# Performance work log

Measured on AMD Instinct MI355X. Metric: run time of the kernel, lower is better.

Reference implementation:

```python
import jax, jax.numpy as jnp
import numpy as np

N = 50000
IN_CH = 256
HID = 256
E = 800000


def setup_inputs() -> dict:
    key = jax.random.key(0)
    ks = jax.random.split(key, 12)
    s = 1.0 / np.sqrt(HID)
    return {
        "x": jax.random.normal(ks[0], (N, IN_CH), jnp.float32),
        "edge_index": jax.random.randint(ks[1], (2, E), 0, N, dtype=jnp.int64),
        "prev_embedding": jax.random.normal(ks[2], (N, HID), jnp.float32),
        "W1": jax.random.normal(ks[3], (IN_CH, HID), jnp.float32) / np.sqrt(IN_CH),
        "b1": jnp.zeros((HID,), jnp.float32),
        "W2": jax.random.normal(ks[4], (HID, HID), jnp.float32) * s,
        "b2": jnp.zeros((HID,), jnp.float32),
        "gWw": jax.random.normal(ks[5], (HID, HID), jnp.float32) * s,
        "gWb": jnp.zeros((HID,), jnp.float32),
        "gUw": jax.random.normal(ks[6], (HID, HID), jnp.float32) * s,
        "gUb": jnp.zeros((HID,), jnp.float32),
    }


def _gcn_conv(x, W, b, src, dst, norm):
    # PyG GCNConv: h = x @ W; out[i] = sum_j norm_ij * h[j]; + bias
    h = x @ W
    msg = h[src] * norm[:, None]  # [E+N, H]
    out = jax.ops.segment_sum(msg, dst, num_segments=N)
    return out + b


def _norm_and_loops(edge_index):
    loop = jnp.arange(N, dtype=edge_index.dtype)
    src = jnp.concatenate([edge_index[0], loop])
    dst = jnp.concatenate([edge_index[1], loop])
    deg = jax.ops.segment_sum(jnp.ones_like(dst, dtype=jnp.float32), dst, num_segments=N)
    dinv = jnp.where(deg > 0, jax.lax.rsqrt(deg), 0.0)
    norm = dinv[src] * dinv[dst]
    return src, dst, norm


def reference(x, edge_index, prev_embedding, W1, b1, W2, b2, gWw, gWb, gUw, gUb):
    src, dst, norm = _norm_and_loops(edge_index)
    h = jax.nn.relu(_gcn_conv(x, W1, b1, src, dst, norm))
    h_t = _gcn_conv(h, W2, b2, src, dst, norm)
    alpha = jax.nn.sigmoid(h_t @ gWw + gWb + prev_embedding @ gUw + gUb)
    h_tilde = alpha * h_t + (1.0 - alpha) * prev_embedding
    return (h_tilde, h_t)
```

## Files before the change

kernel.cpp:

```cpp
#include <hip/hip_runtime.h>
#include <hip/hip_bf16.h>
#include <math.h>

#define HIDC 256
#define LSTR 40

typedef short short8 __attribute__((ext_vector_type(8)));
typedef float f32x4 __attribute__((ext_vector_type(4)));

__device__ __forceinline__ ushort f2bf_rne(float f) {
    uint u = __float_as_uint(f);
    u += 0x7FFF + ((u >> 16) & 1);
    return (ushort)(u >> 16);
}
__device__ __forceinline__ float bf2f(ushort h) {
    return __uint_as_float(((uint)h) << 16);
}


__global__ void fill_i_kernel(int* __restrict__ p, int v, int n) {
    int i = blockIdx.x * 256 + threadIdx.x;
    if (i < n) p[i] = v;
}

__global__ void deg_kernel(const int* __restrict__ dst, int* __restrict__ deg, int E) {
    int e = blockIdx.x * 256 + threadIdx.x;
    if (e < E) atomicAdd(&deg[dst[e]], 1);
}

__global__ void rsqrt_kernel(const int* __restrict__ deg, float* __restrict__ dinv, int n) {
    int i = blockIdx.x * 256 + threadIdx.x;
    if (i < n) dinv[i] = rsqrtf((float)(deg[i] + 1));
}


__device__ __forceinline__ int block_incl_scan(int v, int tid) {
#pragma unroll
    for (int off = 1; off < 64; off <<= 1) {
        int t = __shfl_up(v, off);
        if ((tid & 63) >= off) v += t;
    }
    __shared__ int wt[4];
    if ((tid & 63) == 63) wt[tid >> 6] = v;
    __syncthreads();
    int wid = tid >> 6;
    for (int w = 0; w < wid; w++) v += wt[w];
    __syncthreads();
    return v;
}

__global__ void scan_a_kernel(const int* __restrict__ deg, int* __restrict__ row_start,
                              int* __restrict__ blocksum, int N) {
    int tid = threadIdx.x;
    int i = blockIdx.x * 256 + tid;
    int v = (i < N) ? deg[i] : 0;
    int incl = block_incl_scan(v, tid);
    if (i < N) row_start[i + 1] = incl;
    if (tid == 255) blocksum[blockIdx.x] = incl;
}

__global__ void scan_b_kernel(int* __restrict__ blocksum, int nb) {
    int tid = threadIdx.x;
    int v = (tid < nb) ? blocksum[tid] : 0;
    int incl = block_incl_scan(v, tid);
    if (tid < nb) blocksum[tid] = incl;
}

__global__ void scan_c_kernel(int* __restrict__ row_start, int* __restrict__ cursor,
                              const int* __restrict__ blocksum, int N) {
    int b = blockIdx.x;
    int i = b * 256 + threadIdx.x;
    int add = (b > 0) ? blocksum[b - 1] : 0;
    if (i < N) {
        int v = row_start[i + 1] + add;
        row_start[i + 1] = v;
        cursor[i + 1] = v;
    }
    if (b == 0 && threadIdx.x == 0) { row_start[0] = 0; cursor[0] = 0; }
}

__global__ void scatter_kernel(const int* __restrict__ src, const int* __restrict__ dst,
                               const float* __restrict__ dinv, int* __restrict__ cursor,
                               int* __restrict__ csr_src, float* __restrict__ csr_w, int E) {
    int e = blockIdx.x * 256 + threadIdx.x;
    if (e < E) {
        int s = src[e], d = dst[e];
        int pos = atomicAdd(&cursor[d], 1);
        csr_src[pos] = s;
        csr_w[pos] = dinv[s] * dinv[d];
    }
}


__global__ void prep_bt_kernel(const float* __restrict__ B, ushort* __restrict__ Bt) {
    int n = blockIdx.x, k = threadIdx.x;
    Bt[n * 256 + k] = f2bf_rne(B[k * 256 + n]);
}

__global__ void prep_gate_bt_kernel(const float* __restrict__ gWw, const float* __restrict__ gUw,
                                    ushort* __restrict__ Bth, ushort* __restrict__ Btl) {
    int n = blockIdx.x, k = threadIdx.x;
    float v1 = gWw[k * 256 + n];
    uint u1 = __float_as_uint(v1);
    Bth[n * 512 + k] = (ushort)(u1 >> 16);
    Btl[n * 512 + k] = f2bf_rne(v1 - __uint_as_float(u1 & 0xFFFF0000u));
    float v2 = gUw[k * 256 + n];
    uint u2 = __float_as_uint(v2);
    Bth[n * 512 + 256 + k] = (ushort)(u2 >> 16);
    Btl[n * 512 + 256 + k] = f2bf_rne(v2 - __uint_as_float(u2 & 0xFFFF0000u));
}


__global__ __launch_bounds__(256, 4) void gemm_bf16_kernel(
    const float* __restrict__ A, const ushort* __restrict__ Bt,
    ushort* __restrict__ C, int M)
{
    __shared__ __align__(16) ushort As[128 * LSTR];
    __shared__ __align__(16) ushort Bs[128 * LSTR];
    const int tl = threadIdx.x;
    const int lane = tl & 63, wave = tl >> 6;
    const int wm = (wave & 1) * 64, wn = (wave >> 1) * 64;
    const int bm = blockIdx.x * 128, bn = blockIdx.y * 128;

    const int ar  = tl >> 1;
    const int akq = (tl & 1) * 16;
    const bool aok = (bm + ar) < M;

    f32x4 acc[4][4] = {};

    for (int k0 = 0; k0 < 256; k0 += 32) {
        {
            const float* ap = A + (size_t)(bm + ar) * HIDC + k0 + akq;
#pragma unroll
            for (int j = 0; j < 4; j++) {
                float4 v = aok ? *(const float4*)(ap + 4 * j) : make_float4(0.f, 0.f, 0.f, 0.f);
                ushort4 h;
                h.x = f2bf_rne(v.x); h.y = f2bf_rne(v.y);
                h.z = f2bf_rne(v.z); h.w = f2bf_rne(v.w);
                *(ushort4*)&As[ar * LSTR + akq + 4 * j] = h;
            }
        }
        {
            const ushort* bp = Bt + (size_t)(bn + ar) * 256 + k0 + akq;
            *(uint4*)&Bs[ar * LSTR + akq]     = *(const uint4*)bp;
            *(uint4*)&Bs[ar * LSTR + akq + 8] = *(const uint4*)(bp + 8);
        }
        __syncthreads();
        const int fr = lane & 15, koff = (lane >> 4) * 8;
        short8 af[4], bfv[4];
#pragma unroll
        for (int t = 0; t < 4; t++) {
            af[t]  = *(const short8*)&As[(wm + t * 16 + fr) * LSTR + koff];
            bfv[t] = *(const short8*)&Bs[(wn + t * 16 + fr) * LSTR + koff];
        }
#pragma unroll
        for (int mt = 0; mt < 4; mt++)
#pragma unroll
            for (int nt = 0; nt < 4; nt++)
                acc[mt][nt] = __builtin_amdgcn_mfma_f32_16x16x32_bf16(af[mt], bfv[nt], acc[mt][nt], 0, 0, 0);
        __syncthreads();
    }

    const int row4 = (lane >> 4) * 4, coln = lane & 15;
#pragma unroll
    for (int mt = 0; mt < 4; mt++)
#pragma unroll
        for (int r = 0; r < 4; r++) {
            int m = bm + wm + mt * 16 + row4 + r;
            if (m < M) {
#pragma unroll
                for (int nt = 0; nt < 4; nt++) {
                    int n = bn + wn + nt * 16 + coln;
                    C[(size_t)m * HIDC + n] = f2bf_rne(acc[mt][nt][r]);
                }
            }
        }
}


__global__ __launch_bounds__(256, 4) void gemm_bf16A_kernel(
    const ushort* __restrict__ A, const ushort* __restrict__ Bt,
    ushort* __restrict__ C, int M)
{
    __shared__ __align__(16) ushort As[128 * LSTR];
    __shared__ __align__(16) ushort Bs[128 * LSTR];
    const int tl = threadIdx.x;
    const int lane = tl & 63, wave = tl >> 6;
    const int wm = (wave & 1) * 64, wn = (wave >> 1) * 64;
    const int bm = blockIdx.x * 128, bn = blockIdx.y * 128;

    const int ar  = tl >> 1;
    const int akq = (tl & 1) * 16;
    const bool aok = (bm + ar) < M;

    f32x4 acc[4][4] = {};

    for (int k0 = 0; k0 < 256; k0 += 32) {
        {
            const ushort* ap = A + (size_t)(bm + ar) * HIDC + k0 + akq;
            uint4 z = make_uint4(0u, 0u, 0u, 0u);
            *(uint4*)&As[ar * LSTR + akq]     = aok ? *(const uint4*)ap       : z;
            *(uint4*)&As[ar * LSTR + akq + 8] = aok ? *(const uint4*)(ap + 8) : z;
        }
        {
            const ushort* bp = Bt + (size_t)(bn + ar) * 256 + k0 + akq;
            *(uint4*)&Bs[ar * LSTR + akq]     = *(const uint4*)bp;
            *(uint4*)&Bs[ar * LSTR + akq + 8] = *(const uint4*)(bp + 8);
        }
        __syncthreads();
        const int fr = lane & 15, koff = (lane >> 4) * 8;
        short8 af[4], bfv[4];
#pragma unroll
        for (int t = 0; t < 4; t++) {
            af[t]  = *(const short8*)&As[(wm + t * 16 + fr) * LSTR + koff];
            bfv[t] = *(const short8*)&Bs[(wn + t * 16 + fr) * LSTR + koff];
        }
#pragma unroll
        for (int mt = 0; mt < 4; mt++)
#pragma unroll
            for (int nt = 0; nt < 4; nt++)
                acc[mt][nt] = __builtin_amdgcn_mfma_f32_16x16x32_bf16(af[mt], bfv[nt], acc[mt][nt], 0, 0, 0);
        __syncthreads();
    }

    const int row4 = (lane >> 4) * 4, coln = lane & 15;
#pragma unroll
    for (int mt = 0; mt < 4; mt++)
#pragma unroll
        for (int r = 0; r < 4; r++) {
            int m = bm + wm + mt * 16 + row4 + r;
            if (m < M) {
#pragma unroll
                for (int nt = 0; nt < 4; nt++) {
                    int n = bn + wn + nt * 16 + coln;
                    C[(size_t)m * HIDC + n] = f2bf_rne(acc[mt][nt][r]);
                }
            }
        }
}


__global__ __launch_bounds__(256, 4) void gate_kernel(
    const float* __restrict__ ht, const float* __restrict__ prev,
    const ushort* __restrict__ Bth, const ushort* __restrict__ Btl,
    const float* __restrict__ gWb, const float* __restrict__ gUb,
    float* __restrict__ out, int M)
{
    __shared__ __align__(16) ushort Ash[64 * LSTR];
    __shared__ __align__(16) ushort Asl[64 * LSTR];
    __shared__ __align__(16) ushort Bsh[128 * LSTR];
    __shared__ __align__(16) ushort Bsl[128 * LSTR];
    const int tl = threadIdx.x;
    const int lane = tl & 63, wave = tl >> 6;
    const int wm = (wave & 1) * 32, wn = (wave >> 1) * 64;
    const int bm = blockIdx.x * 64, bn = blockIdx.y * 128;

    const int arA = tl >> 2;
    const int kqA = (tl & 3) * 8;
    const int arB = tl >> 1;
    const int kqB = (tl & 1) * 16;
    const bool aok = (bm + arA) < M;

    f32x4 acc[2][4] = {};

    for (int k0 = 0; k0 < 512; k0 += 32) {
        {
            const float* srcA = (k0 < 256) ? ht : prev;
            const float* ap = srcA + (size_t)(bm + arA) * HIDC + (k0 & 255) + kqA;
            float4 v0 = aok ? *(const float4*)(ap)     : make_float4(0.f, 0.f, 0.f, 0.f);
            float4 v1 = aok ? *(const float4*)(ap + 4) : make_float4(0.f, 0.f, 0.f, 0.f);
            float vv[8] = {v0.x, v0.y, v0.z, v0.w, v1.x, v1.y, v1.z, v1.w};
            ushort hp[8], lp[8];
#pragma unroll
            for (int q = 0; q < 8; q++) {
                uint u = __float_as_uint(vv[q]);
                hp[q] = (ushort)(u >> 16);
                lp[q] = f2bf_rne(vv[q] - __uint_as_float(u & 0xFFFF0000u));
            }
            *(ushort4*)&Ash[arA * LSTR + kqA]     = make_ushort4(hp[0], hp[1], hp[2], hp[3]);
            *(ushort4*)&Ash[arA * LSTR + kqA + 4] = make_ushort4(hp[4], hp[5], hp[6], hp[7]);
            *(ushort4*)&Asl[arA * LSTR + kqA]     = make_ushort4(lp[0], lp[1], lp[2], lp[3]);
            *(ushort4*)&Asl[arA * LSTR + kqA + 4] = make_ushort4(lp[4], lp[5], lp[6], lp[7]);
        }
        {
            const ushort* bph = Bth + (size_t)(bn + arB) * 512 + k0 + kqB;
            const ushort* bpl = Btl + (size_t)(bn + arB) * 512 + k0 + kqB;
            *(uint4*)&Bsh[arB * LSTR + kqB]     = *(const uint4*)bph;
            *(uint4*)&Bsh[arB * LSTR + kqB + 8] = *(const uint4*)(bph + 8);
            *(uint4*)&Bsl[arB * LSTR + kqB]     = *(const uint4*)bpl;
            *(uint4*)&Bsl[arB * LSTR + kqB + 8] = *(const uint4*)(bpl + 8);
        }
        __syncthreads();
        const int fr = lane & 15, koff = (lane >> 4) * 8;
        short8 afh[2], afl[2], bfh[4], bfl[4];
#pragma unroll
        for (int t = 0; t < 2; t++) {
            afh[t] = *(const short8*)&Ash[(wm + t * 16 + fr) * LSTR + koff];
            afl[t] = *(const short8*)&Asl[(wm + t * 16 + fr) * LSTR + koff];
        }
#pragma unroll
        for (int t = 0; t < 4; t++) {
            bfh[t] = *(const short8*)&Bsh[(wn + t * 16 + fr) * LSTR + koff];
            bfl[t] = *(const short8*)&Bsl[(wn + t * 16 + fr) * LSTR + koff];
        }
#pragma unroll
        for (int mt = 0; mt < 2; mt++)
#pragma unroll
            for (int nt = 0; nt < 4; nt++) {
                acc[mt][nt] = __builtin_amdgcn_mfma_f32_16x16x32_bf16(afh[mt], bfh[nt], acc[mt][nt], 0, 0, 0);
                acc[mt][nt] = __builtin_amdgcn_mfma_f32_16x16x32_bf16(afh[mt], bfl[nt], acc[mt][nt], 0, 0, 0);
                acc[mt][nt] = __builtin_amdgcn_mfma_f32_16x16x32_bf16(afl[mt], bfh[nt], acc[mt][nt], 0, 0, 0);
            }
        __syncthreads();
    }

    const int row4 = (lane >> 4) * 4, coln = lane & 15;
#pragma unroll
    for (int mt = 0; mt < 2; mt++)
#pragma unroll
        for (int r = 0; r < 4; r++) {
            int m = bm + wm + mt * 16 + row4 + r;
            if (m < M) {
#pragma unroll
                for (int nt = 0; nt < 4; nt++) {
                    int n = bn + wn + nt * 16 + coln;
                    size_t idx = (size_t)m * HIDC + n;
                    float g = acc[mt][nt][r] + gWb[n] + gUb[n];
                    float alpha = 1.f / (1.f + expf(-g));
                    out[idx] = alpha * ht[idx] + (1.f - alpha) * prev[idx];
                }
            }
        }
}


__global__ __launch_bounds__(256) void csr_agg_kernel(
    const ushort* __restrict__ hm, const int* __restrict__ row_start,
    const int* __restrict__ csr_src, const float* __restrict__ csr_w,
    const float* __restrict__ dinv, const float* __restrict__ bias,
    float* __restrict__ outf, ushort* __restrict__ outb, int do_relu, int N)
{
    const int wave = threadIdx.x >> 6, lane = threadIdx.x & 63;
    const int i = blockIdx.x * 4 + wave;
    if (i >= N) return;
    const int c = lane * 4;

    const float di = dinv[i];
    const float s2 = di * di;
    ushort4 sv = *(const ushort4*)(hm + (size_t)i * HIDC + c);
    float a0 = s2 * bf2f(sv.x), a1 = s2 * bf2f(sv.y);
    float a2 = s2 * bf2f(sv.z), a3 = s2 * bf2f(sv.w);

    const int b0 = row_start[i], b1 = row_start[i + 1];
    int t = b0;
    for (; t + 4 <= b1; t += 4) {
        int   i0 = csr_src[t],     i1 = csr_src[t + 1];
        int   i2 = csr_src[t + 2], i3 = csr_src[t + 3];
        float w0 = csr_w[t],       w1 = csr_w[t + 1];
        float w2 = csr_w[t + 2],   w3 = csr_w[t + 3];
        ushort4 v0 = *(const ushort4*)(hm + (size_t)i0 * HIDC + c);
        ushort4 v1 = *(const ushort4*)(hm + (size_t)i1 * HIDC + c);
        ushort4 v2 = *(const ushort4*)(hm + (size_t)i2 * HIDC + c);
        ushort4 v3 = *(const ushort4*)(hm + (size_t)i3 * HIDC + c);
        a0 += w0 * bf2f(v0.x); a1 += w0 * bf2f(v0.y); a2 += w0 * bf2f(v0.z); a3 += w0 * bf2f(v0.w);
        a0 += w1 * bf2f(v1.x); a1 += w1 * bf2f(v1.y); a2 += w1 * bf2f(v1.z); a3 += w1 * bf2f(v1.w);
        a0 += w2 * bf2f(v2.x); a1 += w2 * bf2f(v2.y); a2 += w2 * bf2f(v2.z); a3 += w2 * bf2f(v2.w);
        a0 += w3 * bf2f(v3.x); a1 += w3 * bf2f(v3.y); a2 += w3 * bf2f(v3.z); a3 += w3 * bf2f(v3.w);
    }
    for (; t < b1; ++t) {
        int s_ = csr_src[t];
        float w = csr_w[t];
        ushort4 v = *(const ushort4*)(hm + (size_t)s_ * HIDC + c);
        a0 += w * bf2f(v.x); a1 += w * bf2f(v.y); a2 += w * bf2f(v.z); a3 += w * bf2f(v.w);
    }

    float4 bb = *(const float4*)(bias + c);
    a0 += bb.x; a1 += bb.y; a2 += bb.z; a3 += bb.w;
    if (do_relu) {
        a0 = fmaxf(a0, 0.f); a1 = fmaxf(a1, 0.f);
        a2 = fmaxf(a2, 0.f); a3 = fmaxf(a3, 0.f);
    }
    if (outb) {
        ushort4 o;
        o.x = f2bf_rne(a0); o.y = f2bf_rne(a1);
        o.z = f2bf_rne(a2); o.w = f2bf_rne(a3);
        *(ushort4*)(outb + (size_t)i * HIDC + c) = o;
    } else {
        *(float4*)(outf + (size_t)i * HIDC + c) = make_float4(a0, a1, a2, a3);
    }
}


extern "C" void kernel_launch(void* const* d_in, const int* in_sizes, int n_in,
                              void* d_out, int out_size, void* d_ws, size_t ws_size,
                              hipStream_t stream) {
    const float* x    = (const float*)d_in[0];
    const int*   ei   = (const int*)d_in[1];
    const float* prev = (const float*)d_in[2];
    const float* W1   = (const float*)d_in[3];
    const float* b1   = (const float*)d_in[4];
    const float* W2   = (const float*)d_in[5];
    const float* b2   = (const float*)d_in[6];
    const float* gWw  = (const float*)d_in[7];
    const float* gWb  = (const float*)d_in[8];
    const float* gUw  = (const float*)d_in[9];
    const float* gUb  = (const float*)d_in[10];

    const int N = in_sizes[0] / HIDC;
    const int E = in_sizes[1] / 2;
    const int* src = ei;
    const int* dst = ei + E;

    float* out  = (float*)d_out;
    float* out1 = out;
    float* ht   = out + (size_t)N * HIDC;
    ushort* hbf = (ushort*)out1;

    float* ws = (float*)d_ws;
    size_t o = 0;
    auto take = [&](size_t n) { size_t r = o; o += (n + 63) & ~(size_t)63; return r; };
    float*  dinv    = ws + take(N);
    int*    degi    = (int*)(ws + take(N));
    int*    row_st  = (int*)(ws + take(N + 1));
    int*    cursor  = (int*)(ws + take(N + 1));
    int*    csr_src = (int*)(ws + take(E));
    float*  csr_w   = ws + take(E);
    ushort* Bt1     = (ushort*)(ws + take(256 * 256 / 2));
    ushort* Bt2     = (ushort*)(ws + take(256 * 256 / 2));
    ushort* Bth     = (ushort*)(ws + take(256 * 512 / 2));
    ushort* Btl     = (ushort*)(ws + take(256 * 512 / 2));
    ushort* hm      = (ushort*)(ws + take((size_t)N * HIDC / 2));

    const int nbN = (N + 255) / 256;
    const int nbE = (E + 255) / 256;
    dim3 ggrid((N + 127) / 128, 2);
    dim3 ggridG((N + 63) / 64, 2);
    const int nbAgg = (N + 3) / 4;

    int* blocksum = (int*)csr_w;
    fill_i_kernel<<<nbN, 256, 0, stream>>>(degi, 0, N);
    deg_kernel<<<nbE, 256, 0, stream>>>(dst, degi, E);
    scan_a_kernel<<<nbN, 256, 0, stream>>>(degi, row_st, blocksum, N);
    scan_b_kernel<<<1, 256, 0, stream>>>(blocksum, nbN);
    scan_c_kernel<<<nbN, 256, 0, stream>>>(row_st, cursor, blocksum, N);
    rsqrt_kernel<<<nbN, 256, 0, stream>>>(degi, dinv, N);
    scatter_kernel<<<nbE, 256, 0, stream>>>(src, dst, dinv, cursor, csr_src, csr_w, E);

    prep_bt_kernel<<<256, 256, 0, stream>>>(W1, Bt1);
    prep_bt_kernel<<<256, 256, 0, stream>>>(W2, Bt2);
    prep_gate_bt_kernel<<<256, 256, 0, stream>>>(gWw, gUw, Bth, Btl);

    gemm_bf16_kernel<<<ggrid, 256, 0, stream>>>(x, Bt1, hm, N);
    csr_agg_kernel<<<nbAgg, 256, 0, stream>>>(hm, row_st, csr_src, csr_w, dinv, b1,
                                              nullptr, hbf, 1, N);

    gemm_bf16A_kernel<<<ggrid, 256, 0, stream>>>(hbf, Bt2, hm, N);
    csr_agg_kernel<<<nbAgg, 256, 0, stream>>>(hm, row_st, csr_src, csr_w, dinv, b2,
                                              ht, nullptr, 0, N);

    gate_kernel<<<ggridG, 256, 0, stream>>>(ht, prev, Bth, Btl, gWb, gUb, out1, N);

    (void)n_in; (void)out_size; (void)ws_size;
}
```

Measured before the change: 509.2 us.

## Double-buffer LDS in GEMM kernels and fuse small prep/rsqrt kernels

Both bf16 GEMM kernels now use double-buffered shared memory with register prefetch of the next K-slice, so global loads overlap MFMA work and each iteration needs only one barrier. The rsqrt degree computation is folded into the scan kernel, and the three weight transpose/convert kernels are merged into a single launch, which cuts launch overhead. The larger LDS footprint lowers the launch-bounds occupancy hint from 4 to 3 blocks.

```diff
diff --git a/kernel.cpp b/kernel.cpp
--- a/kernel.cpp
+++ b/kernel.cpp
@@ -16,6 +16,9 @@
 __device__ __forceinline__ float bf2f(ushort h) {
     return __uint_as_float(((uint)h) << 16);
 }
+__device__ __forceinline__ f32x4 MF(short8 a, short8 b, f32x4 c) {
+    return __builtin_amdgcn_mfma_f32_16x16x32_bf16(a, b, c, 0, 0, 0);
+}
 
 
 __global__ void fill_i_kernel(int* __restrict__ p, int v, int n) {
@@ -26,11 +29,6 @@
 __global__ void deg_kernel(const int* __restrict__ dst, int* __restrict__ deg, int E) {
     int e = blockIdx.x * 256 + threadIdx.x;
     if (e < E) atomicAdd(&deg[dst[e]], 1);
-}
-
-__global__ void rsqrt_kernel(const int* __restrict__ deg, float* __restrict__ dinv, int n) {
-    int i = blockIdx.x * 256 + threadIdx.x;
-    if (i < n) dinv[i] = rsqrtf((float)(deg[i] + 1));
 }
 
 
@@ -50,12 +48,15 @@
 }
 
 __global__ void scan_a_kernel(const int* __restrict__ deg, int* __restrict__ row_start,
-                              int* __restrict__ blocksum, int N) {
+                              int* __restrict__ blocksum, float* __restrict__ dinv, int N) {
     int tid = threadIdx.x;
     int i = blockIdx.x * 256 + tid;
     int v = (i < N) ? deg[i] : 0;
     int incl = block_incl_scan(v, tid);
-    if (i < N) row_start[i + 1] = incl;
+    if (i < N) {
+        row_start[i + 1] = incl;
+        dinv[i] = rsqrtf((float)(v + 1));
+    }
     if (tid == 255) blocksum[blockIdx.x] = incl;
 }
 
@@ -92,14 +93,13 @@
 }
 
 
-__global__ void prep_bt_kernel(const float* __restrict__ B, ushort* __restrict__ Bt) {
+__global__ void prep_all_kernel(const float* __restrict__ W1, const float* __restrict__ W2,
+                                const float* __restrict__ gWw, const float* __restrict__ gUw,
+                                ushort* __restrict__ Bt1, ushort* __restrict__ Bt2,
+                                ushort* __restrict__ Bth, ushort* __restrict__ Btl) {
     int n = blockIdx.x, k = threadIdx.x;
-    Bt[n * 256 + k] = f2bf_rne(B[k * 256 + n]);
-}
-
-__global__ void prep_gate_bt_kernel(const float* __restrict__ gWw, const float* __restrict__ gUw,
-                                    ushort* __restrict__ Bth, ushort* __restrict__ Btl) {
-    int n = blockIdx.x, k = threadIdx.x;
+    Bt1[n * 256 + k] = f2bf_rne(W1[k * 256 + n]);
+    Bt2[n * 256 + k] = f2bf_rne(W2[k * 256 + n]);
     float v1 = gWw[k * 256 + n];
     uint u1 = __float_as_uint(v1);
     Bth[n * 512 + k] = (ushort)(u1 >> 16);
@@ -111,12 +111,12 @@
 }
 
 
-__global__ __launch_bounds__(256, 4) void gemm_bf16_kernel(
+__global__ __launch_bounds__(256, 3) void gemm_bf16_kernel(
     const float* __restrict__ A, const ushort* __restrict__ Bt,
     ushort* __restrict__ C, int M)
 {
-    __shared__ __align__(16) ushort As[128 * LSTR];
-    __shared__ __align__(16) ushort Bs[128 * LSTR];
+    __shared__ __align__(16) ushort As[2][128 * LSTR];
+    __shared__ __align__(16) ushort Bs[2][128 * LSTR];
     const int tl = threadIdx.x;
     const int lane = tl & 63, wave = tl >> 6;
     const int wm = (wave & 1) * 64, wn = (wave >> 1) * 64;
@@ -125,40 +125,63 @@
     const int ar  = tl >> 1;
     const int akq = (tl & 1) * 16;
     const bool aok = (bm + ar) < M;
+    const float*  apb = A  + (size_t)(bm + ar) * HIDC + akq;
+    const ushort* bpb = Bt + (size_t)(bn + ar) * 256 + akq;
 
     f32x4 acc[4][4] = {};
-
-    for (int k0 = 0; k0 < 256; k0 += 32) {
-        {
-            const float* ap = A + (size_t)(bm + ar) * HIDC + k0 + akq;
+    const float4 z4 = make_float4(0.f, 0.f, 0.f, 0.f);
+    float4 ra[4]; uint4 rb0, rb1;
+
+#pragma unroll
+    for (int j = 0; j < 4; j++) ra[j] = aok ? *(const float4*)(apb + 4 * j) : z4;
+    rb0 = *(const uint4*)(bpb);
+    rb1 = *(const uint4*)(bpb + 8);
+#pragma unroll
+    for (int j = 0; j < 4; j++) {
+        ushort4 h;
+        h.x = f2bf_rne(ra[j].x); h.y = f2bf_rne(ra[j].y);
+        h.z = f2bf_rne(ra[j].z); h.w = f2bf_rne(ra[j].w);
+        *(ushort4*)&As[0][ar * LSTR + akq + 4 * j] = h;
+    }
+    *(uint4*)&Bs[0][ar * LSTR + akq]     = rb0;
+    *(uint4*)&Bs[0][ar * LSTR + akq + 8] = rb1;
+    __syncthreads();
+
+    const int fr = lane & 15, koff = (lane >> 4) * 8;
+    int cur = 0;
+#pragma unroll
+    for (int kq = 0; kq < 8; kq++) {
+        if (kq + 1 < 8) {
+#pragma unroll
+            for (int j = 0; j < 4; j++)
+                ra[j] = aok ? *(const float4*)(apb + (kq + 1) * 32 + 4 * j) : z4;
+            rb0 = *(const uint4*)(bpb + (kq + 1) * 32);
+            rb1 = *(const uint4*)(bpb + (kq + 1) * 32 + 8);
+        }
+        short8 af[4], bfv[4];
+#pragma unroll
+        for (int t = 0; t < 4; t++) {
+            af[t]  = *(const short8*)&As[cur][(wm + t * 16 + fr) * LSTR + koff];
+            bfv[t] = *(const short8*)&Bs[cur][(wn + t * 16 + fr) * LSTR + koff];
+        }
+#pragma unroll
+        for (int mt = 0; mt < 4; mt++)
+#pragma unroll
+            for (int nt = 0; nt < 4; nt++)
+                acc[mt][nt] = MF(af[mt], bfv[nt], acc[mt][nt]);
+        if (kq + 1 < 8) {
 #pragma unroll
             for (int j = 0; j < 4; j++) {
-                float4 v = aok ? *(const float4*)(ap + 4 * j) : make_float4(0.f, 0.f, 0.f, 0.f);
                 ushort4 h;
-                h.x = f2bf_rne(v.x); h.y = f2bf_rne(v.y);
-                h.z = f2bf_rne(v.z); h.w = f2bf_rne(v.w);
-                *(ushort4*)&As[ar * LSTR + akq + 4 * j] = h;
+                h.x = f2bf_rne(ra[j].x); h.y = f2bf_rne(ra[j].y);
+                h.z = f2bf_rne(ra[j].z); h.w = f2bf_rne(ra[j].w);
+                *(ushort4*)&As[cur ^ 1][ar * LSTR + akq + 4 * j] = h;
             }
-        }
-        {
-            const ushort* bp = Bt + (size_t)(bn + ar) * 256 + k0 + akq;
-            *(uint4*)&Bs[ar * LSTR + akq]     = *(const uint4*)bp;
-            *(uint4*)&Bs[ar * LSTR + akq + 8] = *(const uint4*)(bp + 8);
-        }
-        __syncthreads();
-        const int fr = lane & 15, koff = (lane >> 4) * 8;
-        short8 af[4], bfv[4];
-#pragma unroll
-        for (int t = 0; t < 4; t++) {
-            af[t]  = *(const short8*)&As[(wm + t * 16 + fr) * LSTR + koff];
-            bfv[t] = *(const short8*)&Bs[(wn + t * 16 + fr) * LSTR + koff];
-        }
-#pragma unroll
-        for (int mt = 0; mt < 4; mt++)
-#pragma unroll
-            for (int nt = 0; nt < 4; nt++)
-                acc[mt][nt] = __builtin_amdgcn_mfma_f32_16x16x32_bf16(af[mt], bfv[nt], acc[mt][nt], 0, 0, 0);
-        __syncthreads();
+            *(uint4*)&Bs[cur ^ 1][ar * LSTR + akq]     = rb0;
+            *(uint4*)&Bs[cur ^ 1][ar * LSTR + akq + 8] = rb1;
+            __syncthreads();
+            cur ^= 1;
+        }
     }
 
     const int row4 = (lane >> 4) * 4, coln = lane & 15;
@@ -178,12 +201,12 @@
 }
 
 
-__global__ __launch_bounds__(256, 4) void gemm_bf16A_kernel(
+__global__ __launch_bounds__(256, 3) void gemm_bf16A_kernel(
     const ushort* __restrict__ A, const ushort* __restrict__ Bt,
     ushort* __restrict__ C, int M)
 {
-    __shared__ __align__(16) ushort As[128 * LSTR];
-    __shared__ __align__(16) ushort Bs[128 * LSTR];
+    __shared__ __align__(16) ushort As[2][128 * LSTR];
+    __shared__ __align__(16) ushort Bs[2][128 * LSTR];
     const int tl = threadIdx.x;
     const int lane = tl & 63, wave = tl >> 6;
     const int wm = (wave & 1) * 64, wn = (wave >> 1) * 64;
@@ -192,35 +215,52 @@
     const int ar  = tl >> 1;
     const int akq = (tl & 1) * 16;
     const bool aok = (bm + ar) < M;
+    const ushort* apb = A  + (size_t)(bm + ar) * HIDC + akq;
+    const ushort* bpb = Bt + (size_t)(bn + ar) * 256 + akq;
 
     f32x4 acc[4][4] = {};
-
-    for (int k0 = 0; k0 < 256; k0 += 32) {
-        {
-            const ushort* ap = A + (size_t)(bm + ar) * HIDC + k0 + akq;
-            uint4 z = make_uint4(0u, 0u, 0u, 0u);
-            *(uint4*)&As[ar * LSTR + akq]     = aok ? *(const uint4*)ap       : z;
-            *(uint4*)&As[ar * LSTR + akq + 8] = aok ? *(const uint4*)(ap + 8) : z;
-        }
-        {
-            const ushort* bp = Bt + (size_t)(bn + ar) * 256 + k0 + akq;
-            *(uint4*)&Bs[ar * LSTR + akq]     = *(const uint4*)bp;
-            *(uint4*)&Bs[ar * LSTR + akq + 8] = *(const uint4*)(bp + 8);
-        }
-        __syncthreads();
-        const int fr = lane & 15, koff = (lane >> 4) * 8;
+    const uint4 z = make_uint4(0u, 0u, 0u, 0u);
+    uint4 ua0, ua1, rb0, rb1;
+
+    ua0 = aok ? *(const uint4*)(apb)     : z;
+    ua1 = aok ? *(const uint4*)(apb + 8) : z;
+    rb0 = *(const uint4*)(bpb);
+    rb1 = *(const uint4*)(bpb + 8);
+    *(uint4*)&As[0][ar * LSTR + akq]     = ua0;
+    *(uint4*)&As[0][ar * LSTR + akq + 8] = ua1;
+    *(uint4*)&Bs[0][ar * LSTR + akq]     = rb0;
+    *(uint4*)&Bs[0][ar * LSTR + akq + 8] = rb1;
+    __syncthreads();
+
+    const int fr = lane & 15, koff = (lane >> 4) * 8;
+    int cur = 0;
+#pragma unroll
+    for (int kq = 0; kq < 8; kq++) {
+        if (kq + 1 < 8) {
+            ua0 = aok ? *(const uint4*)(apb + (kq + 1) * 32)     : z;
+            ua1 = aok ? *(const uint4*)(apb + (kq + 1) * 32 + 8) : z;
+            rb0 = *(const uint4*)(bpb + (kq + 1) * 32);
+            rb1 = *(const uint4*)(bpb + (kq + 1) * 32 + 8);
+        }
         short8 af[4], bfv[4];
 #pragma unroll
         for (int t = 0; t < 4; t++) {
-            af[t]  = *(const short8*)&As[(wm + t * 16 + fr) * LSTR + koff];
-            bfv[t] = *(const short8*)&Bs[(wn + t * 16 + fr) * LSTR + koff];
+            af[t]  = *(const short8*)&As[cur][(wm + t * 16 + fr) * LSTR + koff];
+            bfv[t] = *(const short8*)&Bs[cur][(wn + t * 16 + fr) * LSTR + koff];
         }
 #pragma unroll
         for (int mt = 0; mt < 4; mt++)
 #pragma unroll
             for (int nt = 0; nt < 4; nt++)
-                acc[mt][nt] = __builtin_amdgcn_mfma_f32_16x16x32_bf16(af[mt], bfv[nt], acc[mt][nt], 0, 0, 0);
-        __syncthreads();
+                acc[mt][nt] = MF(af[mt], bfv[nt], acc[mt][nt]);
+        if (kq + 1 < 8) {
+            *(uint4*)&As[cur ^ 1][ar * LSTR + akq]     = ua0;
+            *(uint4*)&As[cur ^ 1][ar * LSTR + akq + 8] = ua1;
+            *(uint4*)&Bs[cur ^ 1][ar * LSTR + akq]     = rb0;
+            *(uint4*)&Bs[cur ^ 1][ar * LSTR + akq + 8] = rb1;
+            __syncthreads();
+            cur ^= 1;
+        }
     }
 
     const int row4 = (lane >> 4) * 4, coln = lane & 15;
@@ -440,15 +480,12 @@
     int* blocksum = (int*)csr_w;
     fill_i_kernel<<<nbN, 256, 0, stream>>>(degi, 0, N);
     deg_kernel<<<nbE, 256, 0, stream>>>(dst, degi, E);
-    scan_a_kernel<<<nbN, 256, 0, stream>>>(degi, row_st, blocksum, N);
+    scan_a_kernel<<<nbN, 256, 0, stream>>>(degi, row_st, blocksum, dinv, N);
     scan_b_kernel<<<1, 256, 0, stream>>>(blocksum, nbN);
     scan_c_kernel<<<nbN, 256, 0, stream>>>(row_st, cursor, blocksum, N);
-    rsqrt_kernel<<<nbN, 256, 0, stream>>>(degi, dinv, N);
     scatter_kernel<<<nbE, 256, 0, stream>>>(src, dst, dinv, cursor, csr_src, csr_w, E);
 
-    prep_bt_kernel<<<256, 256, 0, stream>>>(W1, Bt1);
-    prep_bt_kernel<<<256, 256, 0, stream>>>(W2, Bt2);
-    prep_gate_bt_kernel<<<256, 256, 0, stream>>>(gWw, gUw, Bth, Btl);
+    prep_all_kernel<<<256, 256, 0, stream>>>(W1, W2, gWw, gUw, Bt1, Bt2, Bth, Btl);
 
     gemm_bf16_kernel<<<ggrid, 256, 0, stream>>>(x, Bt1, hm, N);
     csr_agg_kernel<<<nbAgg, 256, 0, stream>>>(hm, row_st, csr_src, csr_w, dinv, b1,
```

Result: slower. 537.5 us (+5.6%).
